# Kernel optimization log

Hardware: AMD Instinct MI355X
Metric: run time of the kernel (lower is better)

Reference implementation:

```python
import jax, jax.numpy as jnp
import numpy as np

N = 50000      # nodes
E = 800000     # edges
D_IN = 128
D_OUT = 128
R = 8          # relation types
EPS = 1e-12    # F.normalize eps


def setup_inputs() -> dict:
    key = jax.random.key(0)
    ks = jax.random.split(key, 10)
    s_in = 1.0 / np.sqrt(D_IN)
    s_out = 1.0 / np.sqrt(D_OUT)
    return {
        "x": jax.random.normal(ks[0], (N, D_IN), jnp.float32),
        "W1": jax.random.normal(ks[1], (R, D_IN, D_OUT), jnp.float32) * s_in,
        "loopW1": jax.random.normal(ks[2], (D_IN, D_OUT), jnp.float32) * s_in,
        "b1": jax.random.normal(ks[3], (D_OUT,), jnp.float32) * 0.01,
        "W2": jax.random.normal(ks[4], (R, D_OUT, D_OUT), jnp.float32) * s_out,
        "loopW2": jax.random.normal(ks[5], (D_OUT, D_OUT), jnp.float32) * s_out,
        "b2": jax.random.normal(ks[6], (D_OUT,), jnp.float32) * 0.01,
        "src": jax.random.randint(ks[7], (E,), 0, N),
        "dst": jax.random.randint(ks[8], (E,), 0, N),
        "etypes": jax.random.randint(ks[9], (E,), 0, R),
    }


def rel_layer(x, src, dst, etypes, W, loopW, b):
    # transform every node by every relation: [R, N, D_out]
    xw = jnp.einsum('ni,rio->rno', x, W)
    # gather per-edge messages: [E, D_out]
    msg = xw[etypes, src]
    # scatter-add to destination nodes
    agg = jax.ops.segment_sum(msg, dst, num_segments=x.shape[0])
    # self-loop + bias (DGL RelGraphConv defaults)
    return agg + x @ loopW + b


def reference(x, W1, loopW1, b1, W2, loopW2, b2, src, dst, etypes):
    h = jax.nn.relu(rel_layer(x, src, dst, etypes, W1, loopW1, b1))
    h = rel_layer(h, src, dst, etypes, W2, loopW2, b2)
    # F.normalize: row-wise L2, eps=1e-12
    nrm = jnp.maximum(jnp.linalg.norm(h, axis=1, keepdims=True), EPS)
    return h / nrm
```

## Files before the change

kernel.cpp:

```cpp
#include <hip/hip_runtime.h>
#include <hip/hip_bf16.h>

#define D 128
#define CH 4096
#define BM 16

typedef unsigned int u32;
typedef unsigned short u16;
typedef __attribute__((ext_vector_type(8))) short s16x8;
typedef __attribute__((ext_vector_type(4))) float f32x4;
typedef __attribute__((ext_vector_type(2))) float f32x2;
typedef __attribute__((ext_vector_type(2))) u32 u32x2;

__device__ __forceinline__ float bf2f(u16 u) {
    union { u32 u; float f; } v; v.u = ((u32)u) << 16; return v.f;
}
__device__ __forceinline__ u16 f2bf(float f) {
    union { float f; u32 u; } v; v.f = f;
    return (u16)((v.u + 0x7fffu + ((v.u >> 16) & 1u)) >> 16);
}
__device__ __forceinline__ u32 pack_bf2(float a, float b) {
    __hip_bfloat162 t = __float22bfloat162_rn(make_float2(a, b));
    union { __hip_bfloat162 t; u32 u; } v; v.t = t; return v.u;
}
__device__ __forceinline__ void unpack2(u32 u, float& lo, float& hi) {
    union { u32 u; float f; } a, b;
    a.u = u << 16; b.u = u & 0xffff0000u;
    lo = a.f; hi = b.f;
}

__global__ void detect_dtype(const u16* __restrict__ x, int* __restrict__ flag,
                             int* __restrict__ gcnt, int nbuck) {
    __shared__ int cnt;
    if (threadIdx.x == 0) cnt = 0;
    __syncthreads();
    if ((int)threadIdx.x < nbuck) gcnt[threadIdx.x] = 0;
    u16 u = x[2 * threadIdx.x];
    int e = (u >> 7) & 0xFF;
    if (e >= 96 && e <= 150) atomicAdd(&cnt, 1);
    __syncthreads();
    if (threadIdx.x == 0) *flag = (cnt >= 128) ? 0 : 1;
}

__global__ __launch_bounds__(256)
void to_bf16_x(const float4* __restrict__ xin, u32x2* __restrict__ xout,
               long long n4, const int* __restrict__ flag)
{
    if (*flag == 0) return;
    long long i = (long long)blockIdx.x * 256 + threadIdx.x;
    if (i >= n4) return;
    float4 v = xin[i];
    u32x2 o;
    o[0] = pack_bf2(v.x, v.y);
    o[1] = pack_bf2(v.z, v.w);
    xout[i] = o;
}

__global__ __launch_bounds__(256)
void csr_count(const int* __restrict__ dst, int* __restrict__ gcnt, int E, int nbuck) {
    __shared__ int scnt[256];
    int tid = threadIdx.x;
    scnt[tid] = 0;
    __syncthreads();
    int base = blockIdx.x * CH;
#pragma unroll
    for (int it = 0; it < CH / 256; ++it) {
        int e = base + it * 256 + tid;
        if (e < E) atomicAdd(&scnt[dst[e] >> 8], 1);
    }
    __syncthreads();
    if (tid < nbuck && scnt[tid] > 0) atomicAdd(&gcnt[tid], scnt[tid]);
}

__global__ __launch_bounds__(256)
void csr_scan(const int* __restrict__ gcnt, int* __restrict__ bstart, int* __restrict__ bcur,
              int nbuck, int N_, int E_, int* __restrict__ offs) {
    __shared__ int wpart[4];
    int tid = threadIdx.x, lane = tid & 63, wid = tid >> 6;
    int v = (tid < nbuck) ? gcnt[tid] : 0;
    int s = v;
#pragma unroll
    for (int off = 1; off < 64; off <<= 1) {
        int t = __shfl_up(s, off, 64);
        if (lane >= off) s += t;
    }
    if (lane == 63) wpart[wid] = s;
    __syncthreads();
    int add = 0;
    for (int w = 0; w < wid; ++w) add += wpart[w];
    int excl = add + s - v;
    if (tid <= nbuck) bstart[tid] = excl;
    if (tid < nbuck)  bcur[tid]  = excl;
    if (tid == 0) offs[N_] = E_;
}

__global__ __launch_bounds__(256)
void csr_part(const int* __restrict__ src, const int* __restrict__ dst,
              const int* __restrict__ et, int* __restrict__ bcur,
              u32* __restrict__ ebuf, int E, int N, int nbuck) {
    __shared__ int scnt[256], sbase[256];
    int tid = threadIdx.x;
    scnt[tid] = 0;
    __syncthreads();
    int base = blockIdx.x * CH;
#pragma unroll
    for (int it = 0; it < CH / 256; ++it) {
        int e = base + it * 256 + tid;
        if (e < E) atomicAdd(&scnt[dst[e] >> 8], 1);
    }
    __syncthreads();
    if (tid < nbuck) {
        int c = scnt[tid];
        sbase[tid] = c ? atomicAdd(&bcur[tid], c) : 0;
    }
    __syncthreads();
    scnt[tid] = 0;
    __syncthreads();
#pragma unroll
    for (int it = 0; it < CH / 256; ++it) {
        int e = base + it * 256 + tid;
        if (e >= E) continue;
        int d = dst[e];
        int b = d >> 8;
        int p = sbase[b] + atomicAdd(&scnt[b], 1);
        ebuf[p] = ((u32)(d & 255) << 24) | ((u32)et[e] << 16) | (u32)src[e];
    }
}

__global__ __launch_bounds__(256)
void csr_emit(const u32* __restrict__ ebuf, const int* __restrict__ bstart,
              int* __restrict__ offs, int* __restrict__ rowidx, int N) {
    __shared__ int hist[2048], excl[2048], cur[2048];
    __shared__ int wpart[4];
    int b = blockIdx.x, tid = threadIdx.x;
    int lo = bstart[b], hi = bstart[b + 1];
    for (int i = tid; i < 2048; i += 256) { hist[i] = 0; cur[i] = 0; }
    __syncthreads();
    for (int i = lo + tid; i < hi; i += 256) {
        u32 rec = ebuf[i];
        int key = (int)((rec >> 24) << 3) | (int)((rec >> 16) & 7u);
        atomicAdd(&hist[key], 1);
    }
    __syncthreads();
    int loc[8]; int tsum = 0;
#pragma unroll
    for (int k = 0; k < 8; ++k) { loc[k] = tsum; tsum += hist[tid * 8 + k]; }
    int lane = tid & 63, wid = tid >> 6;
    int s = tsum;
#pragma unroll
    for (int off = 1; off < 64; off <<= 1) {
        int t = __shfl_up(s, off, 64);
        if (lane >= off) s += t;
    }
    if (lane == 63) wpart[wid] = s;
    __syncthreads();
    int add = 0;
    for (int w = 0; w < wid; ++w) add += wpart[w];
    int tex = add + s - tsum;
#pragma unroll
    for (int k = 0; k < 8; ++k) excl[tid * 8 + k] = tex + loc[k];
    int node = (b << 8) + tid;
    if (node < N) offs[node] = lo + tex;
    __syncthreads();
    for (int i = lo + tid; i < hi; i += 256) {
        u32 rec = ebuf[i];
        int key = (int)((rec >> 24) << 3) | (int)((rec >> 16) & 7u);
        int p = lo + excl[key] + atomicAdd(&cur[key], 1);
        rowidx[p] = (int)(((rec >> 24) & 31u) << 19) | (int)(rec & 0x7FFFFu);
    }
}

__global__ __launch_bounds__(256)
void build_wt(const void* __restrict__ W1r, const void* __restrict__ lW1r,
              const void* __restrict__ W2r, const void* __restrict__ lW2r,
              const int* __restrict__ flag, int R_, u16* __restrict__ wt)
{
    bool f = (*flag != 0);
    int m = blockIdx.x;
    int layer = m / 9, c = m % 9;
    size_t esz = f ? 4 : 2;
    const char* src;
    if (layer == 0) src = (c < R_) ? ((const char*)W1r + (size_t)c * D * D * esz) : (const char*)lW1r;
    else            src = (c < R_) ? ((const char*)W2r + (size_t)c * D * D * esz) : (const char*)lW2r;
    int tid = threadIdx.x;
    u16* dstp = wt + (size_t)m * 16384;
    for (int i = tid; i < 16384; i += 256) {
        int wvv = i >> 11;
        int ks  = (i >> 9) & 3;
        int ln  = (i >> 3) & 63;
        int j   = i & 7;
        int k   = ks * 32 + (ln >> 4) * 8 + j;
        int col = wvv * 16 + (ln & 15);
        int idx = k * 128 + col;
        dstp[i] = f ? f2bf(((const float*)src)[idx]) : ((const u16*)src)[idx];
    }
}

__global__ __launch_bounds__(512, 8)
void rel_layer_fused(const u16* __restrict__ xc, const u16* __restrict__ xo,
                     const int* __restrict__ offs, const int* __restrict__ rowidx,
                     const u16* __restrict__ wt,
                     const void* __restrict__ bias_raw,
                     const int* __restrict__ flag,
                     int M, int R_, int mode, void* __restrict__ out)
{
    __shared__ u16 As[9 * BM * D];
    const bool f = (*flag != 0);
    const u16* X = f ? xc : xo;

    const int row0 = blockIdx.x * BM;
    const int tid  = threadIdx.x;
    const int lane = tid & 63;
    const int wv   = tid >> 6;
    const int quad = lane >> 4;
    const int l16  = lane & 15;

    if (wv < 4) {
        auto* lds0 = (__attribute__((address_space(3))) char*)As;
        int rl = wv * 4 + quad;
        int rg = row0 + rl; if (rg >= M) rg = M - 1;
        int cg = l16 ^ rl;
        const u16* gp = X + (size_t)rg * D + cg * 8;
        __builtin_amdgcn_global_load_lds(
            (const __attribute__((address_space(1))) void*)gp,
            (__attribute__((address_space(3))) void*)(lds0 + 8 * BM * 256 + wv * 1024),
            16, 0, 0);
    }

    {
        u32* pz = (u32*)As;
        int rbase = wv * 2;
#pragma unroll
        for (int pl = 0; pl < 8; ++pl)
#pragma unroll
            for (int rr = 0; rr < 2; ++rr)
                pz[(pl * BM + rbase + rr) * 64 + lane] = 0;
    }

    {
        const u32* X32 = (const u32*)X;
        u32* plane = (u32*)As;
        int rA = row0 + wv * 2;
        int i0 = rA < M ? rA : M;
        int i1 = rA + 2 < M ? rA + 2 : M;
        int j0 = offs[i0], j1 = offs[i1];
        int key = -1;
        float a0 = 0.f, a1 = 0.f;
        int base = j0;
        while (base < j1) {
            int wlen = j1 - base; if (wlen > 64) wlen = 64;
            int vrec = rowidx[base + (lane < wlen ? lane : wlen - 1)];
            for (int pos = 0; pos < wlen; pos += 16) {
                int nb = wlen - pos; if (nb > 16) nb = 16;
                int sr[16]; u32 g[16];
#pragma unroll
                for (int k = 0; k < 16; ++k)
                    if (k < nb) sr[k] = __builtin_amdgcn_readlane(vrec, pos + k);
#pragma unroll
                for (int k = 0; k < 16; ++k)
                    if (k < nb) g[k] = (X32 + ((u32)(sr[k] & 0xffff) << 6))[lane];
#pragma unroll
                for (int k = 0; k < 16; ++k) {
                    if (k < nb) {
                        int nk = sr[k] >> 16;
                        if (nk != key) {
                            if (key >= 0) {
                                int rl = ((key >> 3) - row0) & 31;
                                int vsw = (((lane >> 2) ^ rl) << 2) | (lane & 3);
                                plane[((key & 7) * BM + rl) * 64 + vsw] = pack_bf2(a0, a1);
                            }
                            key = nk; a0 = 0.f; a1 = 0.f;
                        }
                        float lo_, hi_;
                        unpack2(g[k], lo_, hi_);
                        a0 += lo_; a1 += hi_;
                    }
                }
            }
            base += wlen;
        }
        if (key >= 0) {
            int rl = ((key >> 3) - row0) & 31;
            int vsw = (((lane >> 2) ^ rl) << 2) | (lane & 3);
            plane[((key & 7) * BM + rl) * 64 + vsw] = pack_bf2(a0, a1);
        }
    }

    __syncthreads();

    f32x4 acc = (f32x4)0.f;
    for (int c = 0; c <= R_; ++c) {
        int cidx = (c < R_) ? c : 8;
        const u16* Bt = wt + (size_t)cidx * 16384 + (size_t)wv * 2048 + lane * 8;
        s16x8 bfr[4];
#pragma unroll
        for (int ks = 0; ks < 4; ++ks)
            bfr[ks] = *(const s16x8*)(Bt + ks * 512);
#pragma unroll
        for (int ks = 0; ks < 4; ++ks) {
            int chp = (ks * 4 + quad) ^ l16;
            s16x8 a = *(const s16x8*)(As + (cidx * BM + l16) * D + chp * 8);
            acc = __builtin_amdgcn_mfma_f32_16x16x32_bf16(a, bfr[ks], acc, 0, 0, 0);
        }
    }

    const int col = wv * 16 + l16;
    const float b = f ? ((const float*)bias_raw)[col]
                      : bf2f(((const u16*)bias_raw)[col]);

    if (mode == 0) {
        u32* o = (u32*)out;
#pragma unroll
        for (int i = 0; i < 4; ++i) {
            int r = row0 + quad * 4 + i;
            float v = fmaxf(acc[i] + b, 0.f);
            float vp = __shfl_xor(v, 1, 64);
            if (!(l16 & 1) && r < M)
                o[(size_t)r * 64 + (col >> 1)] = pack_bf2(v, vp);
        }
    } else {
        float v[4];
        float pr[4];
#pragma unroll
        for (int i = 0; i < 4; ++i) {
            v[i] = acc[i] + b;
            float p = v[i] * v[i];
            p += __shfl_xor(p, 1, 64);
            p += __shfl_xor(p, 2, 64);
            p += __shfl_xor(p, 4, 64);
            p += __shfl_xor(p, 8, 64);
            pr[i] = p;
        }
        __syncthreads();
        float* fs = (float*)As;
        if (l16 == 0) {
#pragma unroll
            for (int i = 0; i < 4; ++i) fs[(quad * 4 + i) * 8 + wv] = pr[i];
        }
        __syncthreads();
        if (tid < 16) {
            float s = 0.f;
#pragma unroll
            for (int w = 0; w < 8; ++w) s += fs[tid * 8 + w];
            fs[128 + tid] = 1.f / fmaxf(sqrtf(s), 1e-12f);
        }
        __syncthreads();
#pragma unroll
        for (int i = 0; i < 4; ++i) {
            int rl = quad * 4 + i;
            int r = row0 + rl;
            float sc = fs[128 + rl];
            float a0 = v[i] * sc;
            float ap = __shfl_xor(a0, 1, 64);
            if (!(l16 & 1) && r < M) {
                if (f) {
                    f32x2 w; w[0] = a0; w[1] = ap;
                    ((f32x2*)out)[(size_t)r * 64 + (col >> 1)] = w;
                } else {
                    ((u32*)out)[(size_t)r * 64 + (col >> 1)] = pack_bf2(a0, ap);
                }
            }
        }
    }
}

static inline size_t align256(size_t x) { return (x + 255) & ~(size_t)255; }

extern "C" void kernel_launch(void* const* d_in, const int* in_sizes, int n_in,
                              void* d_out, int out_size, void* d_ws, size_t ws_size,
                              hipStream_t stream)
{
    const void* x_in   = d_in[0];
    const void* W1_in  = d_in[1];
    const void* lW1_in = d_in[2];
    const void* b1_in  = d_in[3];
    const void* W2_in  = d_in[4];
    const void* lW2_in = d_in[5];
    const void* b2_in  = d_in[6];
    const int* src = (const int*)d_in[7];
    const int* dst = (const int*)d_in[8];
    const int* et  = (const int*)d_in[9];

    const int N = in_sizes[0] / D;
    const int E = in_sizes[7];
    const int R = in_sizes[1] / (D * D);
    const int nbuck = (N + 255) >> 8;

    const long long ND = (long long)N * D;

    size_t off = 0;
    auto alloc = [&](size_t bytes) { size_t o = off; off = align256(off + bytes); return o; };
    size_t o_flag = alloc(256);
    size_t o_xc   = alloc((size_t)ND * 2);
    size_t o_h    = alloc((size_t)ND * 2);
    size_t o_offs = alloc((size_t)(N + 1) * 4);
    size_t o_gcnt = alloc(1024);
    size_t o_bst  = alloc(1040 * 4);
    size_t o_bcur = alloc(1024);
    size_t o_ebuf = alloc((size_t)E * 4);
    size_t o_ridx = alloc((size_t)E * 4);
    size_t o_wt   = alloc((size_t)2 * 9 * D * D * 2);
    (void)ws_size;

    char* ws = (char*)d_ws;
    int* flag   = (int*)(ws + o_flag);
    u16* x_c    = (u16*)(ws + o_xc);
    u16* h      = (u16*)(ws + o_h);
    int* offs   = (int*)(ws + o_offs);
    int* gcnt   = (int*)(ws + o_gcnt);
    int* bstart = (int*)(ws + o_bst);
    int* bcur   = (int*)(ws + o_bcur);
    u32* ebuf   = (u32*)(ws + o_ebuf);
    int* rowidx = (int*)(ws + o_ridx);
    u16* wt     = (u16*)(ws + o_wt);

    dim3 blk(256, 1, 1);
    int mb    = (N + BM - 1) / BM;
    int nblkE = (E + CH - 1) / CH;

    detect_dtype<<<dim3(1), blk, 0, stream>>>((const u16*)x_in, flag, gcnt, nbuck);

    long long n4 = ND / 4;
    to_bf16_x<<<dim3((u32)((n4 + 255) / 256)), blk, 0, stream>>>(
        (const float4*)x_in, (u32x2*)x_c, n4, flag);

    build_wt<<<dim3(18), blk, 0, stream>>>(
        W1_in, lW1_in, W2_in, lW2_in, flag, R, wt);

    csr_count<<<dim3(nblkE), blk, 0, stream>>>(dst, gcnt, E, nbuck);
    csr_scan<<<dim3(1), blk, 0, stream>>>(gcnt, bstart, bcur, nbuck, N, E, offs);
    csr_part<<<dim3(nblkE), blk, 0, stream>>>(src, dst, et, bcur, ebuf, E, N, nbuck);
    csr_emit<<<dim3(nbuck), blk, 0, stream>>>(ebuf, bstart, offs, rowidx, N);

    rel_layer_fused<<<dim3(mb), dim3(512), 0, stream>>>(
        x_c, (const u16*)x_in, offs, rowidx, wt,
        b1_in, flag, N, R, 0, h);

    rel_layer_fused<<<dim3(mb), dim3(512), 0, stream>>>(
        h, h, offs, rowidx, wt + (size_t)9 * D * D,
        b2_in, flag, N, R, 1, d_out);
}
```

Before: 284.8 us.

## Merge preprocessing kernels and double-buffer edge gathers in fused layer

New measurement: 346.5 us. 1.22x slower.

```diff
diff --git a/kernel.cpp b/kernel.cpp
--- a/kernel.cpp
+++ b/kernel.cpp
@@ -2,7 +2,7 @@
 #include <hip/hip_bf16.h>
 
 #define D 128
-#define CH 4096
+#define CH 2048
 #define BM 16
 
 typedef unsigned int u32;
@@ -23,11 +23,6 @@
     __hip_bfloat162 t = __float22bfloat162_rn(make_float2(a, b));
     union { __hip_bfloat162 t; u32 u; } v; v.t = t; return v.u;
 }
-__device__ __forceinline__ void unpack2(u32 u, float& lo, float& hi) {
-    union { u32 u; float f; } a, b;
-    a.u = u << 16; b.u = u & 0xffff0000u;
-    lo = a.f; hi = b.f;
-}
 
 __global__ void detect_dtype(const u16* __restrict__ x, int* __restrict__ flag,
                              int* __restrict__ gcnt, int nbuck) {
@@ -43,33 +38,34 @@
 }
 
 __global__ __launch_bounds__(256)
-void to_bf16_x(const float4* __restrict__ xin, u32x2* __restrict__ xout,
-               long long n4, const int* __restrict__ flag)
+void prep1(const float4* __restrict__ xin, u32x2* __restrict__ xout,
+           long long n4, const int* __restrict__ flag,
+           const int* __restrict__ dst, int* __restrict__ gcnt,
+           int E, int nbuck, int nconv)
 {
-    if (*flag == 0) return;
-    long long i = (long long)blockIdx.x * 256 + threadIdx.x;
-    if (i >= n4) return;
-    float4 v = xin[i];
-    u32x2 o;
-    o[0] = pack_bf2(v.x, v.y);
-    o[1] = pack_bf2(v.z, v.w);
-    xout[i] = o;
-}
-
-__global__ __launch_bounds__(256)
-void csr_count(const int* __restrict__ dst, int* __restrict__ gcnt, int E, int nbuck) {
-    __shared__ int scnt[256];
-    int tid = threadIdx.x;
-    scnt[tid] = 0;
-    __syncthreads();
-    int base = blockIdx.x * CH;
-#pragma unroll
-    for (int it = 0; it < CH / 256; ++it) {
-        int e = base + it * 256 + tid;
-        if (e < E) atomicAdd(&scnt[dst[e] >> 8], 1);
-    }
-    __syncthreads();
-    if (tid < nbuck && scnt[tid] > 0) atomicAdd(&gcnt[tid], scnt[tid]);
+    if ((int)blockIdx.x < nconv) {
+        if (*flag == 0) return;
+        long long i = (long long)blockIdx.x * 256 + threadIdx.x;
+        if (i >= n4) return;
+        float4 v = xin[i];
+        u32x2 o;
+        o[0] = pack_bf2(v.x, v.y);
+        o[1] = pack_bf2(v.z, v.w);
+        xout[i] = o;
+    } else {
+        __shared__ int scnt[256];
+        int tid = threadIdx.x;
+        scnt[tid] = 0;
+        __syncthreads();
+        int base = (blockIdx.x - nconv) * CH;
+#pragma unroll
+        for (int it = 0; it < CH / 256; ++it) {
+            int e = base + it * 256 + tid;
+            if (e < E) atomicAdd(&scnt[dst[e] >> 8], 1);
+        }
+        __syncthreads();
+        if (tid < nbuck && scnt[tid] > 0) atomicAdd(&gcnt[tid], scnt[tid]);
+    }
 }
 
 __global__ __launch_bounds__(256)
@@ -95,35 +91,61 @@
 }
 
 __global__ __launch_bounds__(256)
-void csr_part(const int* __restrict__ src, const int* __restrict__ dst,
-              const int* __restrict__ et, int* __restrict__ bcur,
-              u32* __restrict__ ebuf, int E, int N, int nbuck) {
-    __shared__ int scnt[256], sbase[256];
-    int tid = threadIdx.x;
-    scnt[tid] = 0;
-    __syncthreads();
-    int base = blockIdx.x * CH;
-#pragma unroll
-    for (int it = 0; it < CH / 256; ++it) {
-        int e = base + it * 256 + tid;
-        if (e < E) atomicAdd(&scnt[dst[e] >> 8], 1);
-    }
-    __syncthreads();
-    if (tid < nbuck) {
-        int c = scnt[tid];
-        sbase[tid] = c ? atomicAdd(&bcur[tid], c) : 0;
-    }
-    __syncthreads();
-    scnt[tid] = 0;
-    __syncthreads();
-#pragma unroll
-    for (int it = 0; it < CH / 256; ++it) {
-        int e = base + it * 256 + tid;
-        if (e >= E) continue;
-        int d = dst[e];
-        int b = d >> 8;
-        int p = sbase[b] + atomicAdd(&scnt[b], 1);
-        ebuf[p] = ((u32)(d & 255) << 24) | ((u32)et[e] << 16) | (u32)src[e];
+void prep2(const int* __restrict__ src, const int* __restrict__ dst,
+           const int* __restrict__ et, int* __restrict__ bcur,
+           u32* __restrict__ ebuf, int E, int N, int nbuck, int nblkE,
+           const void* __restrict__ W1r, const void* __restrict__ lW1r,
+           const void* __restrict__ W2r, const void* __restrict__ lW2r,
+           const int* __restrict__ flag, int R_, u16* __restrict__ wt)
+{
+    if ((int)blockIdx.x < nblkE) {
+        __shared__ int scnt[256], sbase[256];
+        int tid = threadIdx.x;
+        scnt[tid] = 0;
+        __syncthreads();
+        int base = blockIdx.x * CH;
+#pragma unroll
+        for (int it = 0; it < CH / 256; ++it) {
+            int e = base + it * 256 + tid;
+            if (e < E) atomicAdd(&scnt[dst[e] >> 8], 1);
+        }
+        __syncthreads();
+        if (tid < nbuck) {
+            int c = scnt[tid];
+            sbase[tid] = c ? atomicAdd(&bcur[tid], c) : 0;
+        }
+        __syncthreads();
+        scnt[tid] = 0;
+        __syncthreads();
+#pragma unroll
+        for (int it = 0; it < CH / 256; ++it) {
+            int e = base + it * 256 + tid;
+            if (e >= E) continue;
+            int d = dst[e];
+            int b = d >> 8;
+            int p = sbase[b] + atomicAdd(&scnt[b], 1);
+            ebuf[p] = ((u32)(d & 255) << 24) | ((u32)et[e] << 16) | (u32)src[e];
+        }
+    } else {
+        bool f = (*flag != 0);
+        int m = blockIdx.x - nblkE;
+        int layer = m / 9, c = m % 9;
+        size_t esz = f ? 4 : 2;
+        const char* sp;
+        if (layer == 0) sp = (c < R_) ? ((const char*)W1r + (size_t)c * D * D * esz) : (const char*)lW1r;
+        else            sp = (c < R_) ? ((const char*)W2r + (size_t)c * D * D * esz) : (const char*)lW2r;
+        int tid = threadIdx.x;
+        u16* dstp = wt + (size_t)m * 16384;
+        for (int i = tid; i < 16384; i += 256) {
+            int wvv = i >> 11;
+            int ks  = (i >> 9) & 3;
+            int ln  = (i >> 3) & 63;
+            int j   = i & 7;
+            int k   = ks * 32 + (ln >> 4) * 8 + j;
+            int col = wvv * 16 + (ln & 15);
+            int idx = k * 128 + col;
+            dstp[i] = f ? f2bf(((const float*)sp)[idx]) : ((const u16*)sp)[idx];
+        }
     }
 }
 
@@ -167,32 +189,6 @@
         int key = (int)((rec >> 24) << 3) | (int)((rec >> 16) & 7u);
         int p = lo + excl[key] + atomicAdd(&cur[key], 1);
         rowidx[p] = (int)(((rec >> 24) & 31u) << 19) | (int)(rec & 0x7FFFFu);
-    }
-}
-
-__global__ __launch_bounds__(256)
-void build_wt(const void* __restrict__ W1r, const void* __restrict__ lW1r,
-              const void* __restrict__ W2r, const void* __restrict__ lW2r,
-              const int* __restrict__ flag, int R_, u16* __restrict__ wt)
-{
-    bool f = (*flag != 0);
-    int m = blockIdx.x;
-    int layer = m / 9, c = m % 9;
-    size_t esz = f ? 4 : 2;
-    const char* src;
-    if (layer == 0) src = (c < R_) ? ((const char*)W1r + (size_t)c * D * D * esz) : (const char*)lW1r;
-    else            src = (c < R_) ? ((const char*)W2r + (size_t)c * D * D * esz) : (const char*)lW2r;
-    int tid = threadIdx.x;
-    u16* dstp = wt + (size_t)m * 16384;
-    for (int i = tid; i < 16384; i += 256) {
-        int wvv = i >> 11;
-        int ks  = (i >> 9) & 3;
-        int ln  = (i >> 3) & 63;
-        int j   = i & 7;
-        int k   = ks * 32 + (ln >> 4) * 8 + j;
-        int col = wvv * 16 + (ln & 15);
-        int idx = k * 128 + col;
-        dstp[i] = f ? f2bf(((const float*)src)[idx]) : ((const u16*)src)[idx];
     }
 }
 
@@ -245,45 +241,62 @@
         int i1 = rA + 2 < M ? rA + 2 : M;
         int j0 = offs[i0], j1 = offs[i1];
         int key = -1;
-        float a0 = 0.f, a1 = 0.f;
+        f32x2 acc2; acc2[0] = 0.f; acc2[1] = 0.f;
+
+#define ISSUE(SR, G, P) do {                                                  \
+    _Pragma("unroll")                                                         \
+    for (int k_ = 0; k_ < 16; ++k_) {                                         \
+        SR[k_] = __builtin_amdgcn_readlane(vrec, (P) + k_);                   \
+        G[k_]  = (X32 + ((u32)(SR[k_] & 0xffff) << 6))[lane];                 \
+    } } while (0)
+
+#define PROC(SR, G, P) do {                                                   \
+    int nb_ = wlen - (P); if (nb_ > 16) nb_ = 16;                             \
+    _Pragma("unroll")                                                         \
+    for (int k_ = 0; k_ < 16; ++k_) {                                         \
+        if (k_ < nb_) {                                                       \
+            int nk_ = SR[k_] >> 16;                                           \
+            if (nk_ != key) {                                                 \
+                if (key >= 0) {                                               \
+                    int rl_ = ((key >> 3) - row0) & 31;                       \
+                    plane[(((key & 7) * BM + rl_) << 6) + (lane ^ (rl_ << 2))]\
+                        = pack_bf2(acc2[0], acc2[1]);                         \
+                }                                                             \
+                key = nk_; acc2[0] = 0.f; acc2[1] = 0.f;                      \
+            }                                                                 \
+            union { u32 u; float f; } lo_, hi_;                               \
+            lo_.u = G[k_] << 16; hi_.u = G[k_] & 0xffff0000u;                 \
+            f32x2 e_; e_[0] = lo_.f; e_[1] = hi_.f;                           \
+            acc2 += e_;                                                       \
+        }                                                                     \
+    } } while (0)
+
         int base = j0;
         while (base < j1) {
             int wlen = j1 - base; if (wlen > 64) wlen = 64;
             int vrec = rowidx[base + (lane < wlen ? lane : wlen - 1)];
-            for (int pos = 0; pos < wlen; pos += 16) {
-                int nb = wlen - pos; if (nb > 16) nb = 16;
-                int sr[16]; u32 g[16];
-#pragma unroll
-                for (int k = 0; k < 16; ++k)
-                    if (k < nb) sr[k] = __builtin_amdgcn_readlane(vrec, pos + k);
-#pragma unroll
-                for (int k = 0; k < 16; ++k)
-                    if (k < nb) g[k] = (X32 + ((u32)(sr[k] & 0xffff) << 6))[lane];
-#pragma unroll
-                for (int k = 0; k < 16; ++k) {
-                    if (k < nb) {
-                        int nk = sr[k] >> 16;
-                        if (nk != key) {
-                            if (key >= 0) {
-                                int rl = ((key >> 3) - row0) & 31;
-                                int vsw = (((lane >> 2) ^ rl) << 2) | (lane & 3);
-                                plane[((key & 7) * BM + rl) * 64 + vsw] = pack_bf2(a0, a1);
-                            }
-                            key = nk; a0 = 0.f; a1 = 0.f;
-                        }
-                        float lo_, hi_;
-                        unpack2(g[k], lo_, hi_);
-                        a0 += lo_; a1 += hi_;
-                    }
+            int sr0[16], sr1[16]; u32 g0[16], g1[16];
+            ISSUE(sr0, g0, 0);
+            if (wlen > 16) ISSUE(sr1, g1, 16);
+            PROC(sr0, g0, 0);
+            if (wlen > 16) {
+                if (wlen > 32) ISSUE(sr0, g0, 32);
+                PROC(sr1, g1, 16);
+                if (wlen > 32) {
+                    if (wlen > 48) ISSUE(sr1, g1, 48);
+                    PROC(sr0, g0, 32);
+                    if (wlen > 48) PROC(sr1, g1, 48);
                 }
             }
             base += wlen;
         }
         if (key >= 0) {
-            int rl = ((key >> 3) - row0) & 31;
-            int vsw = (((lane >> 2) ^ rl) << 2) | (lane & 3);
-            plane[((key & 7) * BM + rl) * 64 + vsw] = pack_bf2(a0, a1);
-        }
+            int rl_ = ((key >> 3) - row0) & 31;
+            plane[(((key & 7) * BM + rl_) << 6) + (lane ^ (rl_ << 2))]
+                = pack_bf2(acc2[0], acc2[1]);
+        }
+#undef ISSUE
+#undef PROC
     }
 
     __syncthreads();
@@ -417,19 +430,20 @@
     dim3 blk(256, 1, 1);
     int mb    = (N + BM - 1) / BM;
     int nblkE = (E + CH - 1) / CH;
+    long long n4 = ND / 4;
+    int nconv = (int)((n4 + 255) / 256);
 
     detect_dtype<<<dim3(1), blk, 0, stream>>>((const u16*)x_in, flag, gcnt, nbuck);
 
-    long long n4 = ND / 4;
-    to_bf16_x<<<dim3((u32)((n4 + 255) / 256)), blk, 0, stream>>>(
-        (const float4*)x_in, (u32x2*)x_c, n4, flag);
-
-    build_wt<<<dim3(18), blk, 0, stream>>>(
+    prep1<<<dim3(nconv + nblkE), blk, 0, stream>>>(
+        (const float4*)x_in, (u32x2*)x_c, n4, flag, dst, gcnt, E, nbuck, nconv);
+
+    csr_scan<<<dim3(1), blk, 0, stream>>>(gcnt, bstart, bcur, nbuck, N, E, offs);
+
+    prep2<<<dim3(nblkE + 18), blk, 0, stream>>>(
+        src, dst, et, bcur, ebuf, E, N, nbuck, nblkE,
         W1_in, lW1_in, W2_in, lW2_in, flag, R, wt);
 
-    csr_count<<<dim3(nblkE), blk, 0, stream>>>(dst, gcnt, E, nbuck);
-    csr_scan<<<dim3(1), blk, 0, stream>>>(gcnt, bstart, bcur, nbuck, N, E, offs);
-    csr_part<<<dim3(nblkE), blk, 0, stream>>>(src, dst, et, bcur, ebuf, E, N, nbuck);
     csr_emit<<<dim3(nbuck), blk, 0, stream>>>(ebuf, bstart, offs, rowidx, N);
 
     rel_layer_fused<<<dim3(mb), dim3(512), 0, stream>>>(
```
